# Kernel tuning notes

Hardware: AMD Instinct MI355X
Metric: run time of the kernel (lower is better)

Reference implementation:

```python
import jax, jax.numpy as jnp
import numpy as np

N, E, W_IN, W_OUT, NUM_CLASS, M = 4096, 5, 512, 128, 16, 1024
NUM_LAYERS, ALPHA, THETA = 64, 0.1, 0.5

def leaky_relu(x):
    return jnp.where(x >= 0, x, 0.01 * x)

def setup_inputs() -> dict:
    key = jax.random.key(0)
    ks = jax.random.split(key, 16)
    u = jax.random.uniform(ks[0], (N, N, E), jnp.float32)
    A = jnp.where(u < 0.01, u, 0.0)
    X = jax.random.normal(ks[1], (N, W_IN), jnp.float32)
    target_x = jax.random.randint(ks[2], (M,), 0, N)
    target = jax.random.randint(ks[3], (M,), 0, NUM_CLASS)
    def xav(k, shape):
        fan_in, fan_out = shape[-2], shape[-1]
        lim = (6.0 / (fan_in + fan_out)) ** 0.5
        return jax.random.uniform(k, shape, jnp.float32, -lim, lim)
    H0 = W_IN + E * W_OUT  # DGCN input width
    return dict(
        A=A, X=X, target_x=target_x, target=target,
        weight=xav(ks[4], (W_IN, W_OUT)),
        attw=xav(ks[5], (1, N)),
        attb=jnp.zeros((1, W_OUT), jnp.float32),
        attq=xav(ks[6], (1, W_OUT)),
        Wg=xav(ks[7], (W_IN, W_IN)), bg=jnp.zeros((W_IN,), jnp.float32),
        W0=xav(ks[8], (H0, W_OUT)), b0=jnp.zeros((W_OUT,), jnp.float32),
        Wconvs=xav(ks[9], (NUM_LAYERS, W_OUT, W_OUT)),
        Wd1=xav(ks[10], (W_OUT, W_OUT)), bd1=jnp.zeros((W_OUT,), jnp.float32),
        W1=xav(ks[11], (W_OUT, W_OUT)), b1=jnp.zeros((W_OUT,), jnp.float32),
        W2=xav(ks[12], (W_OUT, NUM_CLASS)), b2=jnp.zeros((NUM_CLASS,), jnp.float32),
    )

def reference(A, X, target_x, target, weight, attw, attb, attq, Wg, bg, W0, b0,
              Wconvs, Wd1, bd1, W1, b1, W2, b2):
    Ae = jnp.transpose(A, (2, 0, 1))              # [E,N,N]
    I = jnp.eye(N, dtype=A.dtype)
    # gcn_conv feature transform is identical for every edge type (dropout p=0)
    Xw = leaky_relu(leaky_relu(X @ Wg + bg) @ weight)   # [N, w_out]
    # norm(H, add=True): transpose, set diagonal to 1, row-normalize by degree
    Ht = Ae.transpose(0, 2, 1) * (1.0 - I) + I          # [E,N,N]
    deg = Ht.sum(-1)
    dinv = jnp.where(deg > 0, 1.0 / deg, 0.0)
    lgcn = jax.nn.relu(jnp.einsum('enm,md->end', dinv[..., None] * Ht, Xw))  # [E,N,w_out]
    # edge-type attention
    tm = jnp.tanh(jnp.einsum('n,end->ed', attw[0], lgcn) + attb)  # [E,w_out]
    watt = (tm * attq[0]).sum(-1)                                  # [E]
    beta = jax.nn.softmax(watt) * E
    Xcat = (beta[:, None, None] * lgcn).transpose(1, 0, 2).reshape(N, E * W_OUT)
    X_ = jnp.concatenate([Xcat, X], axis=1)       # [N, w_in + E*w_out]
    # DGCN: GCNII stack on binary nonzero pattern of mean adjacency, gcn_norm
    B = (jnp.mean(Ae, 0) != 0).astype(A.dtype)
    Bs = jnp.maximum(B, I)                        # add remaining self-loops
    d = Bs.sum(1)
    dis = jnp.where(d > 0, jax.lax.rsqrt(d), 0.0)
    A_hat = dis[:, None] * Bs * dis[None, :]      # D^-1/2 (B+I) D^-1/2
    x0 = jax.nn.relu(X_ @ W0 + b0)                # [N, w_out]
    betas_l = jnp.log(THETA / jnp.arange(1, NUM_LAYERS + 1, dtype=A.dtype) + 1.0)
    def step(x, inp):
        Wl, bl = inp
        h = A_hat @ x
        h = (1.0 - ALPHA) * h + ALPHA * x0        # initial residual
        x = jax.nn.relu((1.0 - bl) * h + bl * (h @ Wl))  # identity mapping
        return x, None
    x, _ = jax.lax.scan(step, x0, (Wconvs, betas_l))
    Z = leaky_relu(x @ Wd1 + bd1)                 # DGCN lins[1] + outer leaky_relu
    Z = leaky_relu(Z @ W1 + b1)                   # linear1
    y = Z[target_x] @ W2 + b2                     # linear2 on labeled nodes [M,C]
    logp = jax.nn.log_softmax(y, axis=-1)
    loss = -jnp.mean(jnp.take_along_axis(logp, target[:, None], axis=1))
    return loss, y
```

## Files before the change

### kernel.cpp

```cpp
#include <hip/hip_runtime.h>
#include <cstdint>
#include <cmath>

#define NN   4096
#define EE   5
#define WIN  512
#define WOUT 128
#define HH0  1152
#define NLAY 64
#define NCLS 16
#define MT   1024
#define GCAP 96
#define BCAP 320
#define ECAP 48

typedef __attribute__((ext_vector_type(8))) unsigned short ushort8_t;
typedef __attribute__((ext_vector_type(4))) unsigned short ushort4_t;

__device__ inline unsigned short f2bf(float f) {
  unsigned int u = __float_as_uint(f);
  unsigned int r = (u + 0x7FFFu + ((u >> 16) & 1u)) >> 16;
  return (unsigned short)r;
}

__global__ __launch_bounds__(256) void gemm_kernel(
    const float* __restrict__ A, const float* __restrict__ W,
    const float* __restrict__ bias, float* __restrict__ C,
    int Mdim, int Kdim, int Ndim, int act) {
  __shared__ __align__(16) float sA[16][68];
  __shared__ __align__(16) float sW[16][64];
  int tid = threadIdx.x;
  int tx = tid & 15, ty = tid >> 4;
  int row0 = blockIdx.y * 64, col0 = blockIdx.x * 64;
  float acc[4][4] = {};
  int mA = tid >> 2;
  int kA = (tid & 3) << 2;
  int kW = tid >> 4;
  int nW = (tid & 15) << 2;
  for (int k0 = 0; k0 < Kdim; k0 += 16) {
    float4 av = *(const float4*)(A + (size_t)(row0 + mA) * Kdim + k0 + kA);
    float4 wv = *(const float4*)(W + (size_t)(k0 + kW) * Ndim + col0 + nW);
    sA[kA + 0][mA] = av.x;
    sA[kA + 1][mA] = av.y;
    sA[kA + 2][mA] = av.z;
    sA[kA + 3][mA] = av.w;
    *(float4*)&sW[kW][nW] = wv;
    __syncthreads();
#pragma unroll
    for (int kk = 0; kk < 16; kk++) {
      float4 a = *(const float4*)&sA[kk][ty << 2];
      float4 b = *(const float4*)&sW[kk][tx << 2];
      acc[0][0] += a.x * b.x; acc[0][1] += a.x * b.y; acc[0][2] += a.x * b.z; acc[0][3] += a.x * b.w;
      acc[1][0] += a.y * b.x; acc[1][1] += a.y * b.y; acc[1][2] += a.y * b.z; acc[1][3] += a.y * b.w;
      acc[2][0] += a.z * b.x; acc[2][1] += a.z * b.y; acc[2][2] += a.z * b.z; acc[2][3] += a.z * b.w;
      acc[3][0] += a.w * b.x; acc[3][1] += a.w * b.y; acc[3][2] += a.w * b.z; acc[3][3] += a.w * b.w;
    }
    __syncthreads();
  }
#pragma unroll
  for (int i = 0; i < 4; i++) {
    int r = row0 + (ty << 2) + i;
#pragma unroll
    for (int jc = 0; jc < 4; jc++) {
      int c = col0 + (tx << 2) + jc;
      float o = acc[i][jc];
      if (bias) o += bias[c];
      if (act == 1) o = fmaxf(o, 0.f);
      else if (act == 2) o = (o >= 0.f) ? o : 0.01f * o;
      C[(size_t)r * Ndim + c] = o;
    }
  }
}

__global__ __launch_bounds__(256) void scan_rows_kernel(
    const float* __restrict__ A, int* __restrict__ fcnt, int* __restrict__ fidx,
    float* __restrict__ fval, int* __restrict__ bcnt, int* __restrict__ bidx) {
  __shared__ int   lbuf[1024];
  __shared__ int   lcnt;
  __shared__ int   ecnt[EE];
  __shared__ int   en2[EE][ECAP];
  __shared__ float ev[EE][ECAP];
  __shared__ int   rbase;
  __shared__ int   gbase[EE];
  int tid = threadIdx.x;
  int n1 = blockIdx.x >> 2;
  int qb = (blockIdx.x & 3) << 10;
  if (tid == 0) lcnt = 0;
  if (tid < EE) ecnt[tid] = 0;
  __syncthreads();
  const float4* src = (const float4*)(A + ((size_t)n1 * NN + qb) * EE);
  float buf[20];
  float4* bf4 = (float4*)buf;
#pragma unroll
  for (int c = 0; c < 5; c++) bf4[c] = src[tid * 5 + c];
  int n2base = qb + tid * 4;
#pragma unroll
  for (int u = 0; u < 4; u++) {
    int n2 = n2base + u;
    if (n2 == n1) continue;
    bool any = false;
#pragma unroll
    for (int e = 0; e < EE; e++) {
      float v = buf[u * 5 + e];
      if (v != 0.f) {
        any = true;
        int s = atomicAdd(&ecnt[e], 1);
        if (s < ECAP) { en2[e][s] = n2; ev[e][s] = v; }
      }
    }
    if (any) {
      int s = atomicAdd(&lcnt, 1);
      lbuf[s] = n2;
    }
  }
  __syncthreads();
  if (tid == 0) rbase = atomicAdd(&bcnt[n1], lcnt);
  if (tid < EE) gbase[tid] = atomicAdd(&fcnt[tid * NN + n1], min(ecnt[tid], ECAP));
  __syncthreads();
  int c = lcnt, rb = rbase;
  for (int s = tid; s < c; s += 256)
    if (rb + s < BCAP) bidx[(size_t)n1 * BCAP + rb + s] = lbuf[s];
#pragma unroll
  for (int e = 0; e < EE; e++) {
    int ec = min(ecnt[e], ECAP), gb = gbase[e];
    size_t base = ((size_t)e * NN + n1) * GCAP;
    for (int s = tid; s < ec; s += 256) {
      if (gb + s < GCAP) {
        fidx[base + gb + s] = en2[e][s];
        fval[base + gb + s] = ev[e][s];
      }
    }
  }
}

__global__ __launch_bounds__(64) void transpose_kernel(
    const int* __restrict__ fcnt, const int* __restrict__ fidx, const float* __restrict__ fval,
    int* __restrict__ gcnt, int* __restrict__ gidx, float* __restrict__ gval) {
  int id = blockIdx.x;
  int n1 = id & (NN - 1);
  int e  = id >> 12;
  int c = min(fcnt[id], GCAP);
  for (int s = threadIdx.x; s < c; s += 64) {
    int   n2 = fidx[(size_t)id * GCAP + s];
    float v  = fval[(size_t)id * GCAP + s];
    int t = e * NN + n2;
    int slot = atomicAdd(&gcnt[t], 1);
    if (slot < GCAP) {
      gidx[(size_t)t * GCAP + slot] = n1;
      gval[(size_t)t * GCAP + slot] = v;
    }
  }
}

__global__ void dinv_dis_kernel(const int* __restrict__ gcnt, const float* __restrict__ gval,
                                float* __restrict__ dinv, const int* __restrict__ bcnt,
                                float* __restrict__ dis) {
  int t = blockIdx.x * 256 + threadIdx.x;
  if (t < EE * NN) {
    int cnt = min(gcnt[t], GCAP);
    float s = 1.0f;
    for (int k = 0; k < cnt; k++) s += gval[(size_t)t * GCAP + k];
    dinv[t] = 1.0f / s;
  }
  if (t < NN) dis[t] = rsqrtf(1.0f + (float)min(bcnt[t], BCAP));
}

__global__ __launch_bounds__(64) void build_adj_kernel(
    const int* __restrict__ bcnt, const int* __restrict__ bidx,
    const float* __restrict__ dis, float2* __restrict__ adj, int* __restrict__ acnt) {
  int i = blockIdx.x, t = threadIdx.x;
  int cnt = min(bcnt[i], BCAP - 9);
  float di = dis[i];
  for (int s = t; s < cnt; s += 64) {
    int j = bidx[(size_t)i * BCAP + s];
    adj[(size_t)i * BCAP + s] = make_float2(__int_as_float(j), di * dis[j]);
  }
  int pad = (cnt + 8) & ~7;
  if (t == 0) {
    adj[(size_t)i * BCAP + cnt] = make_float2(__int_as_float(i), di * di);
    acnt[i] = pad;
  }
  for (int s = cnt + 1 + t; s < pad; s += 64)
    adj[(size_t)i * BCAP + s] = make_float2(__int_as_float(i), 0.f);
}

__global__ __launch_bounds__(128) void lgcn_kernel(
    const int* __restrict__ gcnt, const int* __restrict__ gidx, const float* __restrict__ gval,
    const float* __restrict__ dinv, const float* __restrict__ Xw, float* __restrict__ lgcn) {
  int i = blockIdx.x, e = blockIdx.y, d = threadIdx.x;
  int t = e * NN + i;
  int cnt = min(gcnt[t], GCAP);
  __shared__ int   sj[GCAP];
  __shared__ float sv[GCAP];
  for (int s = d; s < cnt; s += 128) {
    sj[s] = gidx[(size_t)t * GCAP + s];
    sv[s] = gval[(size_t)t * GCAP + s];
  }
  __syncthreads();
  float acc = Xw[(size_t)i * WOUT + d];
  for (int s = 0; s < cnt; s++) acc += sv[s] * Xw[(size_t)sj[s] * WOUT + d];
  float r = dinv[t] * acc;
  lgcn[(size_t)t * WOUT + d] = fmaxf(r, 0.f);
}

__global__ void att_partial_kernel(const float* __restrict__ lgcn, const float* __restrict__ attw,
                                   float* __restrict__ tm_pre) {
  int e = blockIdx.y, d = threadIdx.x;
  int nbase = blockIdx.x * 128;
  float acc = 0.f;
  for (int k = 0; k < 128; k++) {
    int n = nbase + k;
    acc += attw[n] * lgcn[((size_t)(e * NN + n)) * WOUT + d];
  }
  atomicAdd(&tm_pre[e * WOUT + d], acc);
}

__global__ void att_final_kernel(const float* __restrict__ tm_pre, const float* __restrict__ attb,
                                 const float* __restrict__ attq, float* __restrict__ beta) {
  int lane = threadIdx.x;
  __shared__ float sw[EE];
  for (int e = 0; e < EE; e++) {
    float v = 0.f;
    for (int d = lane; d < WOUT; d += 64) {
      float tmv = tanhf(tm_pre[e * WOUT + d] + attb[d]);
      v += tmv * attq[d];
    }
    for (int off = 32; off; off >>= 1) v += __shfl_down(v, off, 64);
    if (lane == 0) sw[e] = v;
  }
  __syncthreads();
  if (lane == 0) {
    float mx = sw[0];
    for (int e = 1; e < EE; e++) mx = fmaxf(mx, sw[e]);
    float se = 0.f, ex[EE];
    for (int e = 0; e < EE; e++) { ex[e] = expf(sw[e] - mx); se += ex[e]; }
    for (int e = 0; e < EE; e++) beta[e] = ex[e] / se * (float)EE;
  }
}

__global__ void xcat_kernel(const float* __restrict__ lgcn, const float* __restrict__ X,
                            const float* __restrict__ beta, float* __restrict__ Xc) {
  int idx = blockIdx.x * 256 + threadIdx.x;
  const int total = NN * HH0;
  for (; idx < total; idx += gridDim.x * 256) {
    int n = idx / HH0, c = idx - n * HH0;
    float v;
    if (c < EE * WOUT) {
      int e = c >> 7, d = c & 127;
      v = beta[e] * lgcn[((size_t)(e * NN + n)) * WOUT + d];
    } else {
      v = X[(size_t)n * WIN + (c - EE * WOUT)];
    }
    Xc[idx] = v;
  }
}

__global__ __launch_bounds__(256) void x_to_bf16_kernel(
    const float* __restrict__ x, unsigned short* __restrict__ xb) {
  int idx = blockIdx.x * 256 + threadIdx.x;
  float4 a = ((const float4*)x)[idx * 2];
  float4 b = ((const float4*)x)[idx * 2 + 1];
  unsigned short o[8] = {f2bf(a.x), f2bf(a.y), f2bf(a.z), f2bf(a.w),
                         f2bf(b.x), f2bf(b.y), f2bf(b.z), f2bf(b.w)};
  *(ushort8_t*)&xb[idx * 8] = *(ushort8_t*)o;
}

__global__ __launch_bounds__(512) void gcnii_layer_kernel(
    const float2* __restrict__ adj, const int* __restrict__ acnt,
    const unsigned short* __restrict__ xb, const float* __restrict__ x0,
    const float* __restrict__ Wl, float bl,
    float* __restrict__ xout_f32, unsigned short* __restrict__ xb_out, int write_f32) {
  __shared__ float sh2[128][17];
  int t = threadIdx.x;
  int r = t >> 5, g = t & 31;
  int i = blockIdx.x * 16 + r;
  int cnt = acnt[i];
  const float2* ai = adj + (size_t)i * BCAP;
  const unsigned short* xg = xb + (g << 2);
  float4 acc = {0.f, 0.f, 0.f, 0.f};
  for (int s = 0; s < cnt; s += 8) {
#pragma unroll
    for (int u = 0; u < 8; u++) {
      float2 a = ai[s + u];
      int j = __float_as_int(a.x);
      ushort4_t v = *(const ushort4_t*)(xg + ((size_t)j << 7));
      acc.x = fmaf(a.y, __uint_as_float((unsigned)v.x << 16), acc.x);
      acc.y = fmaf(a.y, __uint_as_float((unsigned)v.y << 16), acc.y);
      acc.z = fmaf(a.y, __uint_as_float((unsigned)v.z << 16), acc.z);
      acc.w = fmaf(a.y, __uint_as_float((unsigned)v.w << 16), acc.w);
    }
  }
  float4 xv = *(const float4*)&x0[((size_t)i << 7) + (g << 2)];
  float4 h;
  h.x = 0.9f * acc.x + 0.1f * xv.x;
  h.y = 0.9f * acc.y + 0.1f * xv.y;
  h.z = 0.9f * acc.z + 0.1f * xv.z;
  h.w = 0.9f * acc.w + 0.1f * xv.w;
  sh2[(g << 2) + 0][r] = h.x;
  sh2[(g << 2) + 1][r] = h.y;
  sh2[(g << 2) + 2][r] = h.z;
  sh2[(g << 2) + 3][r] = h.w;
  __syncthreads();
  float o0 = 0.f, o1 = 0.f, o2 = 0.f, o3 = 0.f;
  const float* wp = Wl + (g << 2);
  for (int k = 0; k < WOUT; k++) {
    float aa = sh2[k][r];
    float4 w = *(const float4*)(wp + (k << 7));
    o0 = fmaf(aa, w.x, o0);
    o1 = fmaf(aa, w.y, o1);
    o2 = fmaf(aa, w.z, o2);
    o3 = fmaf(aa, w.w, o3);
  }
  float c1 = 1.f - bl;
  float y0 = fmaxf(c1 * h.x + bl * o0, 0.f);
  float y1 = fmaxf(c1 * h.y + bl * o1, 0.f);
  float y2 = fmaxf(c1 * h.z + bl * o2, 0.f);
  float y3 = fmaxf(c1 * h.w + bl * o3, 0.f);
  ushort4_t ov;
  ov.x = f2bf(y0); ov.y = f2bf(y1); ov.z = f2bf(y2); ov.w = f2bf(y3);
  *(ushort4_t*)(xb_out + ((size_t)i << 7) + (g << 2)) = ov;
  if (write_f32) {
    float4 yv = {y0, y1, y2, y3};
    *(float4*)&xout_f32[((size_t)i << 7) + (g << 2)] = yv;
  }
}

__global__ __launch_bounds__(256) void head_kernel(
    const float* __restrict__ Z, const int* __restrict__ txv, const int* __restrict__ tgt,
    const float* __restrict__ W2, const float* __restrict__ b2,
    float* __restrict__ out_y, float* __restrict__ lossp) {
  int tid = threadIdx.x;
  int mr = tid >> 4, c = tid & 15;
  int m = blockIdx.x * 16 + mr;
  const float* zr = Z + (size_t)txv[m] * WOUT;
  float acc = b2[c];
  for (int k = 0; k < WOUT; k++) acc += zr[k] * W2[k * NCLS + c];
  out_y[(size_t)m * NCLS + c] = acc;
  float mx = acc;
  for (int off = 8; off; off >>= 1) mx = fmaxf(mx, __shfl_xor(mx, off, 16));
  float ex = expf(acc - mx);
  float se = ex;
  for (int off = 8; off; off >>= 1) se += __shfl_xor(se, off, 16);
  float lse = mx + logf(se);
  float contrib = (c == tgt[m]) ? (lse - acc) : 0.f;
  __shared__ float red[256];
  red[tid] = contrib;
  __syncthreads();
  for (int stp = 128; stp; stp >>= 1) {
    if (tid < stp) red[tid] += red[tid + stp];
    __syncthreads();
  }
  if (tid == 0) lossp[blockIdx.x] = red[0];
}

__global__ void loss_final_kernel(const float* __restrict__ lossp, float* __restrict__ out_loss) {
  int lane = threadIdx.x;
  float v = (lane < 64) ? lossp[lane] : 0.f;
  for (int off = 32; off; off >>= 1) v += __shfl_down(v, off, 64);
  if (lane == 0) out_loss[0] = v / (float)MT;
}

extern "C" void kernel_launch(void* const* d_in, const int* in_sizes, int n_in,
                              void* d_out, int out_size, void* d_ws, size_t ws_size,
                              hipStream_t stream) {
  const float* A      = (const float*)d_in[0];
  const float* X      = (const float*)d_in[1];
  const int*   txv    = (const int*)d_in[2];
  const int*   tgt    = (const int*)d_in[3];
  const float* weight = (const float*)d_in[4];
  const float* attw   = (const float*)d_in[5];
  const float* attb   = (const float*)d_in[6];
  const float* attq   = (const float*)d_in[7];
  const float* Wg     = (const float*)d_in[8];
  const float* bg     = (const float*)d_in[9];
  const float* W0     = (const float*)d_in[10];
  const float* b0     = (const float*)d_in[11];
  const float* Wconvs = (const float*)d_in[12];
  const float* Wd1    = (const float*)d_in[13];
  const float* bd1    = (const float*)d_in[14];
  const float* W1     = (const float*)d_in[15];
  const float* b1     = (const float*)d_in[16];
  const float* W2     = (const float*)d_in[17];
  const float* b2     = (const float*)d_in[18];

  float* ws  = (float*)d_ws;
  int*   wsi = (int*)d_ws;

  const size_t O_GCNT  = 0;
  const size_t O_BCNT  = 20480;
  const size_t O_FCNT  = 24576;
  const size_t O_DINV  = 45056;
  const size_t O_DIS   = 65536;
  const size_t O_TMPRE = 69632;
  const size_t O_BETA  = 70272;
  const size_t O_LOSSP = 70288;
  const size_t O_GIDX  = 71680;
  const size_t O_GVAL  = O_GIDX + 1966080;
  const size_t O_FIDX  = O_GVAL + 1966080;
  const size_t O_FVAL  = O_FIDX + 1966080;
  const size_t O_BIDX  = O_FVAL + 1966080;
  const size_t O_LGCN  = O_BIDX + 1310720;
  const size_t O_XW    = O_LGCN + 2621440;
  const size_t O_X0    = O_XW   + 524288;
  const size_t O_XA    = O_X0   + 524288;
  const size_t O_XB    = O_XA   + 524288;
  const size_t O_ADJ   = O_XB   + 524288;
  const size_t O_XB0   = O_ADJ  + 2621440;
  const size_t O_XB1   = O_XB0  + 262144;
  const size_t O_ACNT  = O_XB1  + 262144;
  const size_t O_T1    = O_FVAL;
  const size_t O_XCAT  = O_GIDX;

  hipMemsetAsync(ws + O_GCNT, 0, 45056 * 4, stream);
  hipMemsetAsync(ws + O_TMPRE, 0, 640 * 4, stream);

  dim3 blk(256);
  gemm_kernel<<<dim3(WIN / 64, NN / 64), blk, 0, stream>>>(X, Wg, bg, ws + O_T1, NN, WIN, WIN, 2);
  gemm_kernel<<<dim3(WOUT / 64, NN / 64), blk, 0, stream>>>(ws + O_T1, weight, nullptr, ws + O_XW, NN, WIN, WOUT, 2);
  scan_rows_kernel<<<NN * 4, 256, 0, stream>>>(A, wsi + O_FCNT, wsi + O_FIDX, ws + O_FVAL,
                                               wsi + O_BCNT, wsi + O_BIDX);
  transpose_kernel<<<EE * NN, 64, 0, stream>>>(wsi + O_FCNT, wsi + O_FIDX, ws + O_FVAL,
                                               wsi + O_GCNT, wsi + O_GIDX, ws + O_GVAL);
  dinv_dis_kernel<<<80, 256, 0, stream>>>(wsi + O_GCNT, ws + O_GVAL, ws + O_DINV,
                                          wsi + O_BCNT, ws + O_DIS);
  build_adj_kernel<<<NN, 64, 0, stream>>>(wsi + O_BCNT, wsi + O_BIDX, ws + O_DIS,
                                          (float2*)(ws + O_ADJ), wsi + O_ACNT);
  lgcn_kernel<<<dim3(NN, EE), 128, 0, stream>>>(wsi + O_GCNT, wsi + O_GIDX, ws + O_GVAL,
                                                ws + O_DINV, ws + O_XW, ws + O_LGCN);
  att_partial_kernel<<<dim3(32, EE), 128, 0, stream>>>(ws + O_LGCN, attw, ws + O_TMPRE);
  att_final_kernel<<<1, 64, 0, stream>>>(ws + O_TMPRE, attb, attq, ws + O_BETA);
  xcat_kernel<<<4096, 256, 0, stream>>>(ws + O_LGCN, X, ws + O_BETA, ws + O_XCAT);
  gemm_kernel<<<dim3(WOUT / 64, NN / 64), blk, 0, stream>>>(ws + O_XCAT, W0, b0, ws + O_X0, NN, HH0, WOUT, 1);
  x_to_bf16_kernel<<<256, 256, 0, stream>>>(ws + O_X0, (unsigned short*)(ws + O_XB0));
  for (int l = 0; l < NLAY; l++) {
    float bl = logf(0.5f / (float)(l + 1) + 1.0f);
    const unsigned short* xin = (const unsigned short*)(ws + ((l & 1) ? O_XB1 : O_XB0));
    unsigned short* xout = (unsigned short*)(ws + ((l & 1) ? O_XB0 : O_XB1));
    gcnii_layer_kernel<<<NN / 16, 512, 0, stream>>>(
        (const float2*)(ws + O_ADJ), wsi + O_ACNT, xin, ws + O_X0,
        Wconvs + (size_t)l * WOUT * WOUT, bl, ws + O_XA, xout, (l == NLAY - 1) ? 1 : 0);
  }
  gemm_kernel<<<dim3(WOUT / 64, NN / 64), blk, 0, stream>>>(ws + O_XA, Wd1, bd1, ws + O_XB, NN, WOUT, WOUT, 2);
  gemm_kernel<<<dim3(WOUT / 64, NN / 64), blk, 0, stream>>>(ws + O_XB, W1, b1, ws + O_X0, NN, WOUT, WOUT, 2);
  head_kernel<<<MT / 16, 256, 0, stream>>>(ws + O_X0, txv, tgt, W2, b2,
                                           (float*)d_out + 1, ws + O_LOSSP);
  loss_final_kernel<<<1, 64, 0, stream>>>(ws + O_LOSSP, (float*)d_out);
}
```

Baseline: 2.804 ms.

## Restructure GCNII layer: split neighbor list across two waves per row, bf16 x0

The GCNII layer kernel now uses 2 rows per 256-thread block. Each row's neighbor list is interleaved into two halves processed by separate wavefronts, and partial sums are reduced in shared memory. Adjacency entries store precomputed byte offsets and are read as float4 pairs. Each lane gathers a 4-byte pair of bf16 features. x0 is read from its bf16 copy, which needs a third ping-pong buffer so the original is not overwritten. The dense 128x128 weight product is split by K across the two waves. The aim is more parallelism and memory-level concurrency in the latency-bound sparse gather, at the cost of extra syncs and reading x0 at bf16 precision.

```diff
diff --git a/kernel.cpp b/kernel.cpp
--- a/kernel.cpp
+++ b/kernel.cpp
@@ -13,6 +13,7 @@
 #define GCAP 96
 #define BCAP 320
 #define ECAP 48
+#define HCAP 160
 
 typedef __attribute__((ext_vector_type(8))) unsigned short ushort8_t;
 typedef __attribute__((ext_vector_type(4))) unsigned short ushort4_t;
@@ -167,21 +168,30 @@
 
 __global__ __launch_bounds__(64) void build_adj_kernel(
     const int* __restrict__ bcnt, const int* __restrict__ bidx,
-    const float* __restrict__ dis, float2* __restrict__ adj, int* __restrict__ acnt) {
+    const float* __restrict__ dis, float2* __restrict__ adjh, int* __restrict__ acnt) {
   int i = blockIdx.x, t = threadIdx.x;
-  int cnt = min(bcnt[i], BCAP - 9);
+  int cnt = min(bcnt[i], 299);
   float di = dis[i];
-  for (int s = t; s < cnt; s += 64) {
-    int j = bidx[(size_t)i * BCAP + s];
-    adj[(size_t)i * BCAP + s] = make_float2(__int_as_float(j), di * dis[j]);
-  }
-  int pad = (cnt + 8) & ~7;
-  if (t == 0) {
-    adj[(size_t)i * BCAP + cnt] = make_float2(__int_as_float(i), di * di);
-    acnt[i] = pad;
-  }
-  for (int s = cnt + 1 + t; s < pad; s += 64)
-    adj[(size_t)i * BCAP + s] = make_float2(__int_as_float(i), 0.f);
+  int total = cnt + 1;
+  int pad = (total + 15) & ~15;
+  for (int s = t; s < pad; s += 64) {
+    unsigned off;
+    float w;
+    if (s < cnt) {
+      int j = bidx[(size_t)i * BCAP + s];
+      off = (unsigned)j << 8;
+      w = di * dis[j];
+    } else if (s == cnt) {
+      off = (unsigned)i << 8;
+      w = di * di;
+    } else {
+      off = (unsigned)i << 8;
+      w = 0.f;
+    }
+    adjh[((size_t)i * 2 + (s & 1)) * HCAP + (s >> 1)] =
+        make_float2(__uint_as_float(off), w);
+  }
+  if (t == 0) acnt[i] = pad >> 1;
 }
 
 __global__ __launch_bounds__(128) void lgcn_kernel(
@@ -265,63 +275,71 @@
   *(ushort8_t*)&xb[idx * 8] = *(ushort8_t*)o;
 }
 
-__global__ __launch_bounds__(512) void gcnii_layer_kernel(
-    const float2* __restrict__ adj, const int* __restrict__ acnt,
-    const unsigned short* __restrict__ xb, const float* __restrict__ x0,
+__global__ __launch_bounds__(256) void gcnii_layer_kernel(
+    const float2* __restrict__ adjh, const int* __restrict__ acnt,
+    const unsigned short* __restrict__ xb_in, const unsigned short* __restrict__ x0b,
     const float* __restrict__ Wl, float bl,
     float* __restrict__ xout_f32, unsigned short* __restrict__ xb_out, int write_f32) {
-  __shared__ float sh2[128][17];
+  __shared__ float part[2][2][128];
+  __shared__ float shh[128 * 3];
   int t = threadIdx.x;
-  int r = t >> 5, g = t & 31;
-  int i = blockIdx.x * 16 + r;
-  int cnt = acnt[i];
-  const float2* ai = adj + (size_t)i * BCAP;
-  const unsigned short* xg = xb + (g << 2);
-  float4 acc = {0.f, 0.f, 0.f, 0.f};
-  for (int s = 0; s < cnt; s += 8) {
-#pragma unroll
-    for (int u = 0; u < 8; u++) {
-      float2 a = ai[s + u];
-      int j = __float_as_int(a.x);
-      ushort4_t v = *(const ushort4_t*)(xg + ((size_t)j << 7));
-      acc.x = fmaf(a.y, __uint_as_float((unsigned)v.x << 16), acc.x);
-      acc.y = fmaf(a.y, __uint_as_float((unsigned)v.y << 16), acc.y);
-      acc.z = fmaf(a.y, __uint_as_float((unsigned)v.z << 16), acc.z);
-      acc.w = fmaf(a.y, __uint_as_float((unsigned)v.w << 16), acc.w);
-    }
-  }
-  float4 xv = *(const float4*)&x0[((size_t)i << 7) + (g << 2)];
-  float4 h;
-  h.x = 0.9f * acc.x + 0.1f * xv.x;
-  h.y = 0.9f * acc.y + 0.1f * xv.y;
-  h.z = 0.9f * acc.z + 0.1f * xv.z;
-  h.w = 0.9f * acc.w + 0.1f * xv.w;
-  sh2[(g << 2) + 0][r] = h.x;
-  sh2[(g << 2) + 1][r] = h.y;
-  sh2[(g << 2) + 2][r] = h.z;
-  sh2[(g << 2) + 3][r] = h.w;
-  __syncthreads();
-  float o0 = 0.f, o1 = 0.f, o2 = 0.f, o3 = 0.f;
-  const float* wp = Wl + (g << 2);
-  for (int k = 0; k < WOUT; k++) {
-    float aa = sh2[k][r];
-    float4 w = *(const float4*)(wp + (k << 7));
-    o0 = fmaf(aa, w.x, o0);
-    o1 = fmaf(aa, w.y, o1);
-    o2 = fmaf(aa, w.z, o2);
-    o3 = fmaf(aa, w.w, o3);
-  }
-  float c1 = 1.f - bl;
-  float y0 = fmaxf(c1 * h.x + bl * o0, 0.f);
-  float y1 = fmaxf(c1 * h.y + bl * o1, 0.f);
-  float y2 = fmaxf(c1 * h.z + bl * o2, 0.f);
-  float y3 = fmaxf(c1 * h.w + bl * o3, 0.f);
-  ushort4_t ov;
-  ov.x = f2bf(y0); ov.y = f2bf(y1); ov.z = f2bf(y2); ov.w = f2bf(y3);
-  *(ushort4_t*)(xb_out + ((size_t)i << 7) + (g << 2)) = ov;
-  if (write_f32) {
-    float4 yv = {y0, y1, y2, y3};
-    *(float4*)&xout_f32[((size_t)i << 7) + (g << 2)] = yv;
+  int wv = t >> 6, lane = t & 63;
+  int r = wv & 1, half = wv >> 1;
+  int i0 = blockIdx.x * 2;
+  int i = i0 + r;
+  int nb = acnt[i];
+  const float4* ah = (const float4*)(adjh + ((size_t)i * 2 + half) * HCAP);
+  const char* xB = (const char*)xb_in + lane * 4;
+  float ax = 0.f, ay = 0.f;
+#define NB(OF, WW)                                                      \
+  {                                                                     \
+    unsigned off = __float_as_uint(OF);                                 \
+    unsigned pv = *(const unsigned*)(xB + off);                         \
+    ax = fmaf((WW), __uint_as_float(pv << 16), ax);                     \
+    ay = fmaf((WW), __uint_as_float(pv & 0xffff0000u), ay);             \
+  }
+  for (int s = 0; s < nb; s += 8) {
+    float4 e0 = ah[(s >> 1) + 0];
+    float4 e1 = ah[(s >> 1) + 1];
+    float4 e2 = ah[(s >> 1) + 2];
+    float4 e3 = ah[(s >> 1) + 3];
+    NB(e0.x, e0.y) NB(e0.z, e0.w) NB(e1.x, e1.y) NB(e1.z, e1.w)
+    NB(e2.x, e2.y) NB(e2.z, e2.w) NB(e3.x, e3.y) NB(e3.z, e3.w)
+  }
+#undef NB
+  *(float2*)&part[half][r][lane * 2] = make_float2(ax, ay);
+  __syncthreads();
+  {
+    int r2 = t >> 7, k = t & 127;
+    int ii = i0 + r2;
+    float x0v = __uint_as_float((unsigned)x0b[((size_t)ii << 7) + k] << 16);
+    float hv = 0.9f * (part[0][r2][k] + part[1][r2][k]) + 0.1f * x0v;
+    shh[k * 3 + r2] = hv;
+  }
+  __syncthreads();
+  {
+    int c2 = lane * 2;
+    float ox = 0.f, oy = 0.f;
+    const float* wp = Wl + (half * 64) * WOUT + c2;
+    int kb = half * 64;
+#pragma unroll 8
+    for (int kk = 0; kk < 64; kk++) {
+      float aa = shh[(kb + kk) * 3 + r];
+      float2 w2 = *(const float2*)(wp + kk * WOUT);
+      ox = fmaf(aa, w2.x, ox);
+      oy = fmaf(aa, w2.y, oy);
+    }
+    *(float2*)&part[half][r][c2] = make_float2(ox, oy);
+  }
+  __syncthreads();
+  {
+    int r2 = t >> 7, k = t & 127;
+    int ii = i0 + r2;
+    float o = part[0][r2][k] + part[1][r2][k];
+    float hv = shh[k * 3 + r2];
+    float y = fmaxf((1.f - bl) * hv + bl * o, 0.f);
+    xb_out[((size_t)ii << 7) + k] = f2bf(y);
+    if (write_f32) xout_f32[((size_t)ii << 7) + k] = y;
   }
 }
 
@@ -407,7 +425,8 @@
   const size_t O_ADJ   = O_XB   + 524288;
   const size_t O_XB0   = O_ADJ  + 2621440;
   const size_t O_XB1   = O_XB0  + 262144;
-  const size_t O_ACNT  = O_XB1  + 262144;
+  const size_t O_XB2   = O_XB1  + 262144;
+  const size_t O_ACNT  = O_XB2  + 262144;
   const size_t O_T1    = O_FVAL;
   const size_t O_XCAT  = O_GIDX;
 
@@ -434,10 +453,12 @@
   x_to_bf16_kernel<<<256, 256, 0, stream>>>(ws + O_X0, (unsigned short*)(ws + O_XB0));
   for (int l = 0; l < NLAY; l++) {
     float bl = logf(0.5f / (float)(l + 1) + 1.0f);
-    const unsigned short* xin = (const unsigned short*)(ws + ((l & 1) ? O_XB1 : O_XB0));
-    unsigned short* xout = (unsigned short*)(ws + ((l & 1) ? O_XB0 : O_XB1));
-    gcnii_layer_kernel<<<NN / 16, 512, 0, stream>>>(
-        (const float2*)(ws + O_ADJ), wsi + O_ACNT, xin, ws + O_X0,
+    const unsigned short* xin = (const unsigned short*)(
+        ws + (l == 0 ? O_XB0 : ((l & 1) ? O_XB1 : O_XB2)));
+    unsigned short* xout = (unsigned short*)(ws + ((l & 1) ? O_XB2 : O_XB1));
+    gcnii_layer_kernel<<<NN / 2, 256, 0, stream>>>(
+        (const float2*)(ws + O_ADJ), wsi + O_ACNT, xin,
+        (const unsigned short*)(ws + O_XB0),
         Wconvs + (size_t)l * WOUT * WOUT, bl, ws + O_XA, xout, (l == NLAY - 1) ? 1 : 0);
   }
   gemm_kernel<<<dim3(WOUT / 64, NN / 64), blk, 0, stream>>>(ws + O_XA, Wd1, bd1, ws + O_XB, NN, WOUT, WOUT, 2);
```

Result: slower. 3.088 ms (+10.1%).
